# Kernel tuning notes

Measured on AMD Instinct MI355X. Metric: run time of the kernel, lower is better.

## Reference

```python
import jax, jax.numpy as jnp
import numpy as np

EPS = 1e-6
N_SRC = 100000
N_TAR = 100000
N = N_SRC + N_TAR
DIM = 128
E = 600000
NEG_SLOPE = 0.01  # torch leaky_relu default


def setup_inputs() -> dict:
    key = jax.random.key(0)
    ks = jax.random.split(key, 8)
    x_src = jax.random.normal(ks[0], (N_SRC, DIM), dtype=jnp.float32)
    x_tar = jax.random.normal(ks[1], (N_TAR, DIM), dtype=jnp.float32)
    edge_index = jax.random.randint(ks[2], (2, E), 0, N, dtype=jnp.int64)
    edge_weight = jax.random.uniform(ks[3], (E,), dtype=jnp.float32)
    W_gcn = jax.random.normal(ks[4], (DIM, DIM), dtype=jnp.float32) / np.sqrt(DIM)
    b_gcn = jax.random.normal(ks[5], (DIM,), dtype=jnp.float32) * 0.01
    W_fnn = jax.random.normal(ks[6], (DIM, DIM), dtype=jnp.float32) / np.sqrt(DIM)
    b_fnn = jax.random.normal(ks[7], (DIM,), dtype=jnp.float32) * 0.01
    return dict(x_src=x_src, x_tar=x_tar, edge_index=edge_index,
                edge_weight=edge_weight, W_gcn=W_gcn, b_gcn=b_gcn,
                W_fnn=W_fnn, b_fnn=b_fnn)


def _gcn_conv(x, edge_index, edge_weight, W, b):
    # PyG GCNConv with add_self_loops=True, symmetric normalization.
    row = jnp.concatenate([edge_index[0], jnp.arange(N, dtype=edge_index.dtype)])
    col = jnp.concatenate([edge_index[1], jnp.arange(N, dtype=edge_index.dtype)])
    w = jnp.concatenate([edge_weight, jnp.ones((N,), dtype=edge_weight.dtype)])
    deg = jax.ops.segment_sum(w, col, num_segments=N)
    dinv = jnp.where(deg > 0, jax.lax.rsqrt(deg), 0.0)
    norm = dinv[row] * w * dinv[col]                 # [E+N]
    h = x @ W                                        # [N, D]
    msg = norm[:, None] * h[row]                     # gather + scale
    out = jnp.zeros_like(h).at[col].add(msg)         # scatter-add to targets
    return out + b


def _node_norm(x):
    mean = jnp.mean(x, axis=1, keepdims=True)
    var = jnp.mean((x - mean) ** 2, axis=1, keepdims=True)  # unbiased=False
    return (x - mean) / jnp.sqrt(var + EPS)


def reference(x_src, x_tar, edge_index, edge_weight, W_gcn, b_gcn, W_fnn, b_fnn):
    x = jnp.concatenate([x_src, x_tar], axis=0)      # [N, D]
    # route == 'MIX': GNN branch + FNN branch on the skip copy
    g = _gcn_conv(x, edge_index, edge_weight, W_gcn, b_gcn)
    f = jax.nn.leaky_relu(x @ W_fnn + b_fnn, NEG_SLOPE)  # dropout = identity (eval)
    x = g + f
    x = _node_norm(x)
    x = jax.nn.leaky_relu(x, NEG_SLOPE)
    return x[:N_SRC, :], x[N_SRC:, :]
```

## Files before the change

### kernel.cpp

```cpp
#include <hip/hip_runtime.h>
#include <hip/hip_bf16.h>
#include <cstddef>
#include <cstdint>

#define DIM 128
#define SCAN_CHUNK 2048

typedef __attribute__((ext_vector_type(8))) short short8v;
typedef __attribute__((ext_vector_type(4))) float f32x4;

__device__ __forceinline__ float leaky(float v) {
    return v > 0.0f ? v : 0.01f * v;
}

__device__ __forceinline__ unsigned short f2bf(float f) {
    unsigned u = __builtin_bit_cast(unsigned, f);
    u += 0x7FFF + ((u >> 16) & 1);
    return (unsigned short)(u >> 16);
}

__device__ __forceinline__ unsigned cvt_pk_bf16(float a, float b) {
    unsigned r;
    asm("v_cvt_pk_bf16_f32 %0, %1, %2" : "=v"(r) : "v"(a), "v"(b));
    return r;
}

__device__ __forceinline__ float bf2f_hi(unsigned p) {
    return __builtin_bit_cast(float, p & 0xFFFF0000u);
}
__device__ __forceinline__ float bf2f_lo(unsigned p) {
    return __builtin_bit_cast(float, p << 16);
}

__device__ __forceinline__ void gload_lds16(const float* g, float* lds) {
    __builtin_amdgcn_global_load_lds(
        (const __attribute__((address_space(1))) unsigned int*)g,
        (__attribute__((address_space(3))) unsigned int*)lds, 16, 0, 0);
}

__global__ __launch_bounds__(256)
void init_kernel(const float* __restrict__ Wg, const float* __restrict__ Wf,
                 unsigned short* __restrict__ WgT, unsigned short* __restrict__ WfT,
                 int* __restrict__ cnt, int N) {
    int t = blockIdx.x * 256 + threadIdx.x;
    if (t < N) cnt[t] = 0;
    if (t < 128 * 128) {
        int col = t >> 7, k = t & 127;
        WgT[col * 128 + k] = f2bf(Wg[k * 128 + col]);
        WfT[col * 128 + k] = f2bf(Wf[k * 128 + col]);
    }
}

__global__ __launch_bounds__(256)
void hist_kernel(const int* __restrict__ col, int* __restrict__ cnt, int E) {
    int e = blockIdx.x * blockDim.x + threadIdx.x;
    if (e < E) atomicAdd(&cnt[col[e]], 1);
}

__global__ __launch_bounds__(256)
void scan_block_sums(const int* __restrict__ cnt, int* __restrict__ bsum, int N) {
    __shared__ int sdata[4];
    int base = blockIdx.x * SCAN_CHUNK;
    int s = 0;
    for (int k = threadIdx.x; k < SCAN_CHUNK; k += 256) {
        int idx = base + k;
        s += (idx < N) ? cnt[idx] : 0;
    }
#pragma unroll
    for (int m = 1; m < 64; m <<= 1) s += __shfl_xor(s, m, 64);
    if ((threadIdx.x & 63) == 0) sdata[threadIdx.x >> 6] = s;
    __syncthreads();
    if (threadIdx.x == 0)
        bsum[blockIdx.x] = sdata[0] + sdata[1] + sdata[2] + sdata[3];
}

__global__ __launch_bounds__(128)
void scan_bsum_kernel(int* __restrict__ bsum, int nb) {
    __shared__ int wtot[2];
    int t = threadIdx.x;
    int lane = t & 63;
    int orig = (t < nb) ? bsum[t] : 0;
    int v = orig;
#pragma unroll
    for (int m = 1; m < 64; m <<= 1) {
        int u = __shfl_up(v, m, 64);
        if (lane >= m) v += u;
    }
    if (lane == 63) wtot[t >> 6] = v;
    __syncthreads();
    if (t >= 64) v += wtot[0];
    if (t < nb) bsum[t] = v - orig;
}

__global__ __launch_bounds__(256)
void scan_write_kernel(int* __restrict__ cnt, const int* __restrict__ bsum,
                       int* __restrict__ off, int N) {
    __shared__ int wsum[4];
    int t = threadIdx.x;
    int base = blockIdx.x * SCAN_CHUNK + t * 8;
    int vals[8];
    int local = 0;
#pragma unroll
    for (int k = 0; k < 8; ++k) {
        int idx = base + k;
        int c = (idx < N) ? cnt[idx] : 0;
        vals[k] = local;
        local += c;
    }
    int tsum = local;
    int lane = t & 63;
    int v = tsum;
#pragma unroll
    for (int m = 1; m < 64; m <<= 1) {
        int u = __shfl_up(v, m, 64);
        if (lane >= m) v += u;
    }
    if (lane == 63) wsum[t >> 6] = v;
    __syncthreads();
    int woff = 0;
    for (int i = 0; i < (t >> 6); ++i) woff += wsum[i];
    int texcl = (v - tsum) + woff + bsum[blockIdx.x];
#pragma unroll
    for (int k = 0; k < 8; ++k) {
        int idx = base + k;
        int o = texcl + vals[k];
        if (idx <= N) off[idx] = o;
    }
    __syncthreads();
#pragma unroll
    for (int k = 0; k < 8; ++k) {
        int idx = base + k;
        int o = texcl + vals[k];
        if (idx < N) cnt[idx] = o;
    }
}

__global__ __launch_bounds__(256)
void reorder_kernel(const int* __restrict__ row, const int* __restrict__ col,
                    const float* __restrict__ w, int* __restrict__ cursor,
                    int2* __restrict__ edgeRW, int E) {
    int e = blockIdx.x * blockDim.x + threadIdx.x;
    if (e < E) {
        int c = col[e];
        int pos = atomicAdd(&cursor[c], 1);
        edgeRW[pos] = make_int2(row[e], __builtin_bit_cast(int, w[e]));
    }
}

__global__ __launch_bounds__(256)
void csr_dinv_kernel(const int* __restrict__ off, const int2* __restrict__ edgeRW,
                     float* __restrict__ dinv, int N) {
    int i = blockIdx.x * 256 + threadIdx.x;
    if (i >= N) return;
    int s = off[i], e = off[i + 1];
    float acc = 1.0f;
    for (int j = s; j < e; ++j)
        acc += __builtin_bit_cast(float, edgeRW[j].y);
    dinv[i] = rsqrtf(acc);
}

__global__ __launch_bounds__(512, 4)
void gemm_mfma_kernel(const float* __restrict__ x_src, const float* __restrict__ x_tar,
                      int n_src, int n_total, int ntiles,
                      const unsigned short* __restrict__ WgT,
                      const unsigned short* __restrict__ WfT,
                      const float* __restrict__ bg, const float* __restrict__ bf,
                      const float* __restrict__ dinv,
                      unsigned short* __restrict__ hsb,
                      unsigned short* __restrict__ accb)
{
    __shared__ float Ash[4][32 * 128];
    __shared__ float dinvS[448];

    const int t    = threadIdx.x;
    const int lane = t & 63;
    const int wv   = t >> 6;
    const int h    = wv >> 2;
    const int q    = wv & 3;
    const int lr   = lane & 15;
    const int lk   = lane >> 4;

    const int nb  = gridDim.x;
    const int K   = (ntiles + nb - 1) / nb;
    const int t0  = blockIdx.x * K;
    const int cnt = min(K, ntiles - t0);
    if (cnt <= 0) return;

    if (t < cnt * 32) {
        int gi = t0 * 32 + t;
        if (gi >= n_total) gi = n_total - 1;
        dinvS[t] = dinv[gi];
    }
    asm volatile("s_waitcnt lgkmcnt(0)" ::: "memory");

    short8v wg[4][2], wf[4][2];
#pragma unroll
    for (int ks = 0; ks < 4; ++ks)
#pragma unroll
        for (int nf = 0; nf < 2; ++nf) {
            int col = q * 32 + ((lr >> 2) << 3) + nf * 4 + (lr & 3);
            const size_t bo = (size_t)col * 128 + ks * 32 + lk * 8;
            wg[ks][nf] = *(const short8v*)(WgT + bo);
            wf[ks][nf] = *(const short8v*)(WfT + bo);
        }
    const int cb = q * 32 + lk * 8;
    float4 bgv[2], bfv[2];
#pragma unroll
    for (int nf = 0; nf < 2; ++nf) {
        bgv[nf] = *(const float4*)(bg + cb + nf * 4);
        bfv[nf] = *(const float4*)(bf + cb + nf * 4);
    }

    auto stage = [&](int tl, int buf) {
#pragma unroll
        for (int s = 0; s < 2; ++s) {
            int id  = s * 512 + t;
            int row = id >> 5;
            int cs  = id & 31;
            int c   = cs ^ (row & 15);
            int rg  = tl * 32 + row;
            if (rg >= n_total) rg = n_total - 1;
            const float* xr = (rg < n_src) ? x_src + (size_t)rg * DIM
                                           : x_tar + (size_t)(rg - n_src) * DIM;
            gload_lds16(xr + c * 4, &Ash[buf][(size_t)(s * 512 + wv * 64) * 4]);
        }
    };

    stage(t0, 0);
    if (1 < cnt) stage(t0 + 1, 1);
    if (2 < cnt) stage(t0 + 2, 2);

    const int xrow = h * 16 + lr;
    const int xrs  = xrow & 15;

    for (int it = 0; it < cnt; ++it) {
        if (cnt >= 6) {
            if (it == 0)              asm volatile("s_waitcnt vmcnt(4)"  ::: "memory");
            else if (it == 1)         asm volatile("s_waitcnt vmcnt(6)"  ::: "memory");
            else if (it == 2)         asm volatile("s_waitcnt vmcnt(8)"  ::: "memory");
            else if (it == cnt - 2)   asm volatile("s_waitcnt vmcnt(8)"  ::: "memory");
            else if (it == cnt - 1)   asm volatile("s_waitcnt vmcnt(6)"  ::: "memory");
            else                      asm volatile("s_waitcnt vmcnt(10)" ::: "memory");
        } else {
            asm volatile("s_waitcnt vmcnt(0)" ::: "memory");
        }
        __builtin_amdgcn_sched_barrier(0);
        __builtin_amdgcn_s_barrier();
        __builtin_amdgcn_sched_barrier(0);

        if (it + 3 < cnt) stage(t0 + it + 3, (it + 3) & 3);

        const int cur = it & 3;
        f32x4 accg[2], accf[2];
        accg[0] = (f32x4)0.0f; accg[1] = (f32x4)0.0f;
        accf[0] = (f32x4)0.0f; accf[1] = (f32x4)0.0f;

#pragma unroll
        for (int ks = 0; ks < 4; ++ks) {
            int c0 = ks * 8 + lk * 2;
            float4 q0 = *(const float4*)&Ash[cur][(size_t)(xrow * 32 + ( c0      ^ xrs)) * 4];
            float4 q1 = *(const float4*)&Ash[cur][(size_t)(xrow * 32 + ((c0 + 1) ^ xrs)) * 4];
            union { short8v v; unsigned u[4]; } cv;
            cv.u[0] = cvt_pk_bf16(q0.x, q0.y);
            cv.u[1] = cvt_pk_bf16(q0.z, q0.w);
            cv.u[2] = cvt_pk_bf16(q1.x, q1.y);
            cv.u[3] = cvt_pk_bf16(q1.z, q1.w);
#pragma unroll
            for (int nf = 0; nf < 2; ++nf) {
                accg[nf] = __builtin_amdgcn_mfma_f32_16x16x32_bf16(wg[ks][nf], cv.v, accg[nf], 0, 0, 0);
                accf[nf] = __builtin_amdgcn_mfma_f32_16x16x32_bf16(wf[ks][nf], cv.v, accf[nf], 0, 0, 0);
            }
        }

        const int tile = t0 + it;
        int r = tile * 32 + xrow;
        const bool valid = (r < n_total);
        float dv = dinvS[it * 32 + xrow];

        float hs[8], oo[8];
#pragma unroll
        for (int nf = 0; nf < 2; ++nf)
#pragma unroll
            for (int e = 0; e < 4; ++e) {
                int k = nf * 4 + e;
                hs[k] = dv * accg[nf][e];
                float f = accf[nf][e] + ((const float*)&bfv[nf])[e];
                oo[k] = leaky(f) + ((const float*)&bgv[nf])[e] + dv * hs[k];
            }

        uint4 hp, op;
        hp.x = cvt_pk_bf16(hs[0], hs[1]); hp.y = cvt_pk_bf16(hs[2], hs[3]);
        hp.z = cvt_pk_bf16(hs[4], hs[5]); hp.w = cvt_pk_bf16(hs[6], hs[7]);
        op.x = cvt_pk_bf16(oo[0], oo[1]); op.y = cvt_pk_bf16(oo[2], oo[3]);
        op.z = cvt_pk_bf16(oo[4], oo[5]); op.w = cvt_pk_bf16(oo[6], oo[7]);

        if (valid) {
            *(uint4*)(hsb  + (size_t)r * DIM + cb) = hp;
            *(uint4*)(accb + (size_t)r * DIM + cb) = op;
        }
    }
}

__global__ __launch_bounds__(256)
void gather_norm_kernel(const int* __restrict__ off, const int2* __restrict__ edgeRW,
                        const float* __restrict__ dinv,
                        const unsigned short* __restrict__ hsb,
                        const unsigned short* __restrict__ accb,
                        float* __restrict__ out, int n)
{
    const int wid  = threadIdx.x >> 6;
    const int lane = threadIdx.x & 63;
    const int sub  = lane >> 4;
    const int sl   = lane & 15;
    int i = (blockIdx.x * 4 + wid) * 4 + sub;
    if (i >= n) i = n - 1;

    const int start = off[i];
    const int degc  = off[i + 1] - start;

    int md = degc;
    md = max(md, __shfl_xor(md, 16, 64));
    md = max(md, __shfl_xor(md, 32, 64));

    float s[8];
#pragma unroll
    for (int k = 0; k < 8; ++k) s[k] = 0.0f;

    const unsigned short* gbase = hsb + (size_t)sl * 8;

    int   r0 = 0, r1 = 0;
    float w0 = 0.0f, w1 = 0.0f;
    if (0 < degc) { int2 m = edgeRW[start];     r0 = m.x; w0 = __builtin_bit_cast(float, m.y); }
    if (1 < degc) { int2 m = edgeRW[start + 1]; r1 = m.x; w1 = __builtin_bit_cast(float, m.y); }
    uint4 p0 = *(const uint4*)(gbase + (size_t)r0 * DIM);

    for (int t = 0; t < md; ++t) {
        uint4 p1 = p0;
        if (t + 1 < md)
            p1 = *(const uint4*)(gbase + (size_t)r1 * DIM);
        int r2 = 0; float w2 = 0.0f;
        if (t + 2 < md) {
            if (t + 2 < degc) {
                int2 m = edgeRW[start + t + 2];
                r2 = m.x; w2 = __builtin_bit_cast(float, m.y);
            }
        }
        s[0] += w0 * bf2f_lo(p0.x); s[1] += w0 * bf2f_hi(p0.x);
        s[2] += w0 * bf2f_lo(p0.y); s[3] += w0 * bf2f_hi(p0.y);
        s[4] += w0 * bf2f_lo(p0.z); s[5] += w0 * bf2f_hi(p0.z);
        s[6] += w0 * bf2f_lo(p0.w); s[7] += w0 * bf2f_hi(p0.w);
        p0 = p1;
        r0 = r1; w0 = w1;
        r1 = r2; w1 = w2;
    }

    const float dv = dinv[i];
    uint4 av = *(const uint4*)(accb + (size_t)i * DIM + sl * 8);
    float v[8];
    v[0] = bf2f_lo(av.x) + dv * s[0]; v[1] = bf2f_hi(av.x) + dv * s[1];
    v[2] = bf2f_lo(av.y) + dv * s[2]; v[3] = bf2f_hi(av.y) + dv * s[3];
    v[4] = bf2f_lo(av.z) + dv * s[4]; v[5] = bf2f_hi(av.z) + dv * s[5];
    v[6] = bf2f_lo(av.w) + dv * s[6]; v[7] = bf2f_hi(av.w) + dv * s[7];

    float sum = 0.0f;
#pragma unroll
    for (int k = 0; k < 8; ++k) sum += v[k];
#pragma unroll
    for (int m = 1; m < 16; m <<= 1) sum += __shfl_xor(sum, m, 64);
    const float mean = sum * (1.0f / 128.0f);

    float sq = 0.0f;
#pragma unroll
    for (int k = 0; k < 8; ++k) {
        v[k] -= mean;
        sq += v[k] * v[k];
    }
#pragma unroll
    for (int m = 1; m < 16; m <<= 1) sq += __shfl_xor(sq, m, 64);
    const float rstd = rsqrtf(sq * (1.0f / 128.0f) + 1e-6f);

    float4 o1, o2;
    o1.x = leaky(v[0] * rstd); o1.y = leaky(v[1] * rstd);
    o1.z = leaky(v[2] * rstd); o1.w = leaky(v[3] * rstd);
    o2.x = leaky(v[4] * rstd); o2.y = leaky(v[5] * rstd);
    o2.z = leaky(v[6] * rstd); o2.w = leaky(v[7] * rstd);
    float* op = out + (size_t)i * DIM + sl * 8;
    *(float4*)op       = o1;
    *(float4*)(op + 4) = o2;
}

extern "C" void kernel_launch(void* const* d_in, const int* in_sizes, int n_in,
                              void* d_out, int out_size, void* d_ws, size_t ws_size,
                              hipStream_t stream)
{
    const float* x_src = (const float*)d_in[0];
    const float* x_tar = (const float*)d_in[1];
    const int*   ei    = (const int*)d_in[2];
    const float* ew    = (const float*)d_in[3];
    const float* Wg    = (const float*)d_in[4];
    const float* bg    = (const float*)d_in[5];
    const float* Wf    = (const float*)d_in[6];
    const float* bf    = (const float*)d_in[7];

    const int n_src = in_sizes[0] / DIM;
    const int n_tar = in_sizes[1] / DIM;
    const int N     = n_src + n_tar;
    const int E     = in_sizes[3];

    const int* rowp = ei;
    const int* colp = ei + E;

    char* p = (char*)d_ws;
    float* dinv = (float*)p;  p += (size_t)N * 4;
    int*   cnt  = (int*)p;    p += (size_t)N * 4;
    int*   off  = (int*)p;    p += (size_t)(N + 1) * 4;
    int*   bsum = (int*)p;    p += 160 * 4;
    p = (char*)(((uintptr_t)p + 15) & ~(uintptr_t)15);
    int2*  edgeRW = (int2*)p; p += (size_t)E * 8;
    unsigned short* hsb  = (unsigned short*)p; p += (size_t)N * DIM * 2;
    unsigned short* accb = (unsigned short*)p; p += (size_t)N * DIM * 2;
    unsigned short* WgT  = (unsigned short*)p; p += 128 * 128 * 2;
    unsigned short* WfT  = (unsigned short*)p;

    const int NB = (N + 1 + SCAN_CHUNK - 1) / SCAN_CHUNK;

    init_kernel<<<(N + 255) / 256, 256, 0, stream>>>(Wg, Wf, WgT, WfT, cnt, N);

    hist_kernel<<<(E + 255) / 256, 256, 0, stream>>>(colp, cnt, E);

    scan_block_sums<<<NB, 256, 0, stream>>>(cnt, bsum, N);
    scan_bsum_kernel<<<1, 128, 0, stream>>>(bsum, NB);
    scan_write_kernel<<<NB, 256, 0, stream>>>(cnt, bsum, off, N);

    reorder_kernel<<<(E + 255) / 256, 256, 0, stream>>>(rowp, colp, ew, cnt,
                                                        edgeRW, E);

    csr_dinv_kernel<<<(N + 255) / 256, 256, 0, stream>>>(off, edgeRW, dinv, N);

    const int ntiles = (N + 31) / 32;
    gemm_mfma_kernel<<<512, 512, 0, stream>>>(
        x_src, x_tar, n_src, N, ntiles, WgT, WfT, bg, bf, dinv, hsb, accb);

    gather_norm_kernel<<<(N + 15) / 16, 256, 0, stream>>>(
        off, edgeRW, dinv, hsb, accb, (float*)d_out, N);
}
```

Baseline: 194.4 us.

## Fuse degree computation into GEMM and gather, drop init and dinv kernels

Removes the separate init and csr_dinv kernels: the weight transpose is folded into the histogram kernel, the count reset becomes a memset, and the degree-inverse is recomputed inside the GEMM prologue and inside the gather loop by summing edge weights. The GEMM drops from four to three LDS staging buffers with a two-tile prefetch, so six blocks fit per CU and the grid grows to 768. This cuts kernel launches and the dinv global round trip, at the cost of redundant degree sums and a shallower prefetch pipeline.

```diff
diff --git a/kernel.cpp b/kernel.cpp
--- a/kernel.cpp
+++ b/kernel.cpp
@@ -39,22 +39,16 @@
 }
 
 __global__ __launch_bounds__(256)
-void init_kernel(const float* __restrict__ Wg, const float* __restrict__ Wf,
-                 unsigned short* __restrict__ WgT, unsigned short* __restrict__ WfT,
-                 int* __restrict__ cnt, int N) {
-    int t = blockIdx.x * 256 + threadIdx.x;
-    if (t < N) cnt[t] = 0;
-    if (t < 128 * 128) {
-        int col = t >> 7, k = t & 127;
-        WgT[col * 128 + k] = f2bf(Wg[k * 128 + col]);
-        WfT[col * 128 + k] = f2bf(Wf[k * 128 + col]);
-    }
-}
-
-__global__ __launch_bounds__(256)
-void hist_kernel(const int* __restrict__ col, int* __restrict__ cnt, int E) {
-    int e = blockIdx.x * blockDim.x + threadIdx.x;
-    if (e < E) atomicAdd(&cnt[col[e]], 1);
+void hist_kernel(const int* __restrict__ col, int* __restrict__ cnt, int E,
+                 const float* __restrict__ Wg, const float* __restrict__ Wf,
+                 unsigned short* __restrict__ WgT, unsigned short* __restrict__ WfT) {
+    int gid = blockIdx.x * blockDim.x + threadIdx.x;
+    if (gid < 128 * 128) {
+        int c = gid >> 7, k = gid & 127;
+        WgT[c * 128 + k] = f2bf(Wg[k * 128 + c]);
+        WfT[c * 128 + k] = f2bf(Wf[k * 128 + c]);
+    }
+    if (gid < E) atomicAdd(&cnt[col[gid]], 1);
 }
 
 __global__ __launch_bounds__(256)
@@ -147,30 +141,18 @@
     }
 }
 
-__global__ __launch_bounds__(256)
-void csr_dinv_kernel(const int* __restrict__ off, const int2* __restrict__ edgeRW,
-                     float* __restrict__ dinv, int N) {
-    int i = blockIdx.x * 256 + threadIdx.x;
-    if (i >= N) return;
-    int s = off[i], e = off[i + 1];
-    float acc = 1.0f;
-    for (int j = s; j < e; ++j)
-        acc += __builtin_bit_cast(float, edgeRW[j].y);
-    dinv[i] = rsqrtf(acc);
-}
-
-__global__ __launch_bounds__(512, 4)
+__global__ __launch_bounds__(512, 6)
 void gemm_mfma_kernel(const float* __restrict__ x_src, const float* __restrict__ x_tar,
                       int n_src, int n_total, int ntiles,
+                      const int* __restrict__ off, const int2* __restrict__ edgeRW,
                       const unsigned short* __restrict__ WgT,
                       const unsigned short* __restrict__ WfT,
                       const float* __restrict__ bg, const float* __restrict__ bf,
-                      const float* __restrict__ dinv,
                       unsigned short* __restrict__ hsb,
                       unsigned short* __restrict__ accb)
 {
-    __shared__ float Ash[4][32 * 128];
-    __shared__ float dinvS[448];
+    __shared__ float Ash[3][32 * 128];
+    __shared__ float dinvS[320];
 
     const int t    = threadIdx.x;
     const int lane = t & 63;
@@ -186,12 +168,19 @@
     const int cnt = min(K, ntiles - t0);
     if (cnt <= 0) return;
 
-    if (t < cnt * 32) {
-        int gi = t0 * 32 + t;
+    for (int tt = t; tt < cnt * 32; tt += 512) {
+        int gi = t0 * 32 + tt;
         if (gi >= n_total) gi = n_total - 1;
-        dinvS[t] = dinv[gi];
+        int s0 = off[gi], e0 = off[gi + 1];
+        float a = 1.0f;
+        for (int j = s0; j < e0; ++j)
+            a += __builtin_bit_cast(float, edgeRW[j].y);
+        dinvS[tt] = rsqrtf(a);
     }
     asm volatile("s_waitcnt lgkmcnt(0)" ::: "memory");
+    __builtin_amdgcn_sched_barrier(0);
+    asm volatile("s_waitcnt vmcnt(0)" ::: "memory");
+    __builtin_amdgcn_sched_barrier(0);
 
     short8v wg[4][2], wf[4][2];
 #pragma unroll
@@ -210,6 +199,9 @@
         bgv[nf] = *(const float4*)(bg + cb + nf * 4);
         bfv[nf] = *(const float4*)(bf + cb + nf * 4);
     }
+    __builtin_amdgcn_sched_barrier(0);
+    asm volatile("s_waitcnt vmcnt(0)" ::: "memory");
+    __builtin_amdgcn_sched_barrier(0);
 
     auto stage = [&](int tl, int buf) {
 #pragma unroll
@@ -228,19 +220,17 @@
 
     stage(t0, 0);
     if (1 < cnt) stage(t0 + 1, 1);
-    if (2 < cnt) stage(t0 + 2, 2);
 
     const int xrow = h * 16 + lr;
     const int xrs  = xrow & 15;
 
+    int cur = 0;
     for (int it = 0; it < cnt; ++it) {
-        if (cnt >= 6) {
-            if (it == 0)              asm volatile("s_waitcnt vmcnt(4)"  ::: "memory");
-            else if (it == 1)         asm volatile("s_waitcnt vmcnt(6)"  ::: "memory");
-            else if (it == 2)         asm volatile("s_waitcnt vmcnt(8)"  ::: "memory");
-            else if (it == cnt - 2)   asm volatile("s_waitcnt vmcnt(8)"  ::: "memory");
-            else if (it == cnt - 1)   asm volatile("s_waitcnt vmcnt(6)"  ::: "memory");
-            else                      asm volatile("s_waitcnt vmcnt(10)" ::: "memory");
+        if (cnt >= 3) {
+            if (it == 0)            asm volatile("s_waitcnt vmcnt(2)" ::: "memory");
+            else if (it == 1)       asm volatile("s_waitcnt vmcnt(4)" ::: "memory");
+            else if (it == cnt - 1) asm volatile("s_waitcnt vmcnt(4)" ::: "memory");
+            else                    asm volatile("s_waitcnt vmcnt(6)" ::: "memory");
         } else {
             asm volatile("s_waitcnt vmcnt(0)" ::: "memory");
         }
@@ -248,9 +238,11 @@
         __builtin_amdgcn_s_barrier();
         __builtin_amdgcn_sched_barrier(0);
 
-        if (it + 3 < cnt) stage(t0 + it + 3, (it + 3) & 3);
-
-        const int cur = it & 3;
+        if (it + 2 < cnt) {
+            int b = cur + 2; if (b >= 3) b -= 3;
+            stage(t0 + it + 2, b);
+        }
+
         f32x4 accg[2], accf[2];
         accg[0] = (f32x4)0.0f; accg[1] = (f32x4)0.0f;
         accf[0] = (f32x4)0.0f; accf[1] = (f32x4)0.0f;
@@ -298,12 +290,12 @@
             *(uint4*)(hsb  + (size_t)r * DIM + cb) = hp;
             *(uint4*)(accb + (size_t)r * DIM + cb) = op;
         }
+        ++cur; if (cur == 3) cur = 0;
     }
 }
 
 __global__ __launch_bounds__(256)
 void gather_norm_kernel(const int* __restrict__ off, const int2* __restrict__ edgeRW,
-                        const float* __restrict__ dinv,
                         const unsigned short* __restrict__ hsb,
                         const unsigned short* __restrict__ accb,
                         float* __restrict__ out, int n)
@@ -325,6 +317,7 @@
     float s[8];
 #pragma unroll
     for (int k = 0; k < 8; ++k) s[k] = 0.0f;
+    float sw = 0.0f;
 
     const unsigned short* gbase = hsb + (size_t)sl * 8;
 
@@ -345,6 +338,7 @@
                 r2 = m.x; w2 = __builtin_bit_cast(float, m.y);
             }
         }
+        sw += w0;
         s[0] += w0 * bf2f_lo(p0.x); s[1] += w0 * bf2f_hi(p0.x);
         s[2] += w0 * bf2f_lo(p0.y); s[3] += w0 * bf2f_hi(p0.y);
         s[4] += w0 * bf2f_lo(p0.z); s[5] += w0 * bf2f_hi(p0.z);
@@ -354,7 +348,7 @@
         r1 = r2; w1 = w2;
     }
 
-    const float dv = dinv[i];
+    const float dv = rsqrtf(1.0f + sw);
     uint4 av = *(const uint4*)(accb + (size_t)i * DIM + sl * 8);
     float v[8];
     v[0] = bf2f_lo(av.x) + dv * s[0]; v[1] = bf2f_hi(av.x) + dv * s[1];
@@ -411,7 +405,6 @@
     const int* colp = ei + E;
 
     char* p = (char*)d_ws;
-    float* dinv = (float*)p;  p += (size_t)N * 4;
     int*   cnt  = (int*)p;    p += (size_t)N * 4;
     int*   off  = (int*)p;    p += (size_t)(N + 1) * 4;
     int*   bsum = (int*)p;    p += 160 * 4;
@@ -424,9 +417,10 @@
 
     const int NB = (N + 1 + SCAN_CHUNK - 1) / SCAN_CHUNK;
 
-    init_kernel<<<(N + 255) / 256, 256, 0, stream>>>(Wg, Wf, WgT, WfT, cnt, N);
-
-    hist_kernel<<<(E + 255) / 256, 256, 0, stream>>>(colp, cnt, E);
+    hipMemsetAsync(cnt, 0, (size_t)N * sizeof(int), stream);
+
+    hist_kernel<<<(E + 255) / 256, 256, 0, stream>>>(colp, cnt, E,
+                                                     Wg, Wf, WgT, WfT);
 
     scan_block_sums<<<NB, 256, 0, stream>>>(cnt, bsum, N);
     scan_bsum_kernel<<<1, 128, 0, stream>>>(bsum, NB);
@@ -435,12 +429,11 @@
     reorder_kernel<<<(E + 255) / 256, 256, 0, stream>>>(rowp, colp, ew, cnt,
                                                         edgeRW, E);
 
-    csr_dinv_kernel<<<(N + 255) / 256, 256, 0, stream>>>(off, edgeRW, dinv, N);
-
     const int ntiles = (N + 31) / 32;
-    gemm_mfma_kernel<<<512, 512, 0, stream>>>(
-        x_src, x_tar, n_src, N, ntiles, WgT, WfT, bg, bf, dinv, hsb, accb);
+    gemm_mfma_kernel<<<768, 512, 0, stream>>>(
+        x_src, x_tar, n_src, N, ntiles, off, edgeRW, WgT, WfT, bg, bf,
+        hsb, accb);
 
     gather_norm_kernel<<<(N + 15) / 16, 256, 0, stream>>>(
-        off, edgeRW, dinv, hsb, accb, (float*)d_out, N);
-}
+        off, edgeRW, hsb, accb, (float*)d_out, N);
+}
```

After: 291.1 us. 1.5x slower.
